# Kernel tuning notes

Hardware: AMD Instinct MI355X
Metric: run time of the kernel (lower is better)

The kernel has to match this reference:

```python
import jax, jax.numpy as jnp
import numpy as np

N, E, DIM, EDIM, H, T = 30000, 300000, 64, 16, 3, 6


def setup_inputs() -> dict:
    key = jax.random.key(0)
    ks = jax.random.split(key, 20)
    s = 0.1
    inp = {
        'x': jax.random.normal(ks[0], (N, DIM), jnp.float32),
        'edge_index': jax.random.randint(ks[1], (2, E), 0, N, jnp.int64),
        'edge_attr': jax.random.normal(ks[2], (E, EDIM), jnp.float32),
        # EdgeGATConv params (heads=3, out per head = DIM, concat=False -> head mean)
        'Wg': jax.random.normal(ks[3], (DIM, H * DIM), jnp.float32) * s,
        'bg': jnp.zeros((DIM,), jnp.float32),
        'a_src': jax.random.normal(ks[4], (H, DIM), jnp.float32) * s,
        'a_dst': jax.random.normal(ks[5], (H, DIM), jnp.float32) * s,
        'We': jax.random.normal(ks[6], (EDIM, H * DIM), jnp.float32) * s,
        'a_edge': jax.random.normal(ks[7], (H, DIM), jnp.float32) * s,
        # GRU (1 layer), torch gate order: r, z, n
        'Wih': jax.random.normal(ks[8], (3 * DIM, DIM), jnp.float32) * s,
        'Whh': jax.random.normal(ks[9], (3 * DIM, DIM), jnp.float32) * s,
        'bih': jnp.zeros((3 * DIM,), jnp.float32),
        'bhh': jnp.zeros((3 * DIM,), jnp.float32),
        # NodeLevelBatchNorm per time step
        'gamma': jnp.ones((T, DIM), jnp.float32),
        'beta': jnp.zeros((T, DIM), jnp.float32),
        # final linear: dim*(T+1) -> dim
        'Wlin': jax.random.normal(ks[10], (DIM * (T + 1), DIM), jnp.float32) * s,
        'blin': jnp.zeros((DIM,), jnp.float32),
    }
    return inp


def _edge_gat(x, edge_index, edge_attr, Wg, bg, a_src, a_dst, We, a_edge):
    n = x.shape[0]
    xw = (x @ Wg).reshape(n, H, DIM)                 # [N,H,C]
    ew = (edge_attr @ We).reshape(-1, H, DIM)        # [E,H,C]
    src, dst = edge_index[0], edge_index[1]
    logits = ((xw[src] * a_src).sum(-1)
              + (xw[dst] * a_dst).sum(-1)
              + (ew * a_edge).sum(-1))               # [E,H]
    logits = jax.nn.leaky_relu(logits, 0.2)
    # segment softmax over incoming edges per destination node
    amax = jax.ops.segment_max(logits, dst, num_segments=n)
    amax = jnp.where(jnp.isfinite(amax), amax, 0.0)
    ex = jnp.exp(logits - amax[dst])
    denom = jax.ops.segment_sum(ex, dst, num_segments=n)
    att = ex / (denom[dst] + 1e-16)                  # [E,H]
    agg = jax.ops.segment_sum(xw[src] * att[..., None], dst, num_segments=n)  # [N,H,C]
    return agg.mean(axis=1) + bg                     # concat=False: head mean


def _gru_step(m, h, Wih, Whh, bih, bhh):
    gi = m @ Wih.T + bih
    gh = h @ Whh.T + bhh
    ir, iz, inn = jnp.split(gi, 3, axis=-1)
    hr, hz, hn = jnp.split(gh, 3, axis=-1)
    r = jax.nn.sigmoid(ir + hr)
    z = jax.nn.sigmoid(iz + hz)
    nn_ = jnp.tanh(inn + r * hn)
    return (1.0 - z) * nn_ + z * h


def _node_bn(x, gamma, beta, eps=1e-5):
    mu = x.mean(axis=0)
    var = ((x - mu) ** 2).mean(axis=0)
    return (x - mu) * jax.lax.rsqrt(var + eps) * gamma + beta


def reference(x, edge_index, edge_attr, Wg, bg, a_src, a_dst, We, a_edge,
              Wih, Whh, bih, bhh, gamma, beta, Wlin, blin):
    h = x
    feats = [x]
    for i in range(T):
        m = jax.nn.celu(_edge_gat(x, edge_index, edge_attr, Wg, bg, a_src, a_dst, We, a_edge))
        h = _gru_step(m, h, Wih, Whh, bih, bhh)
        x = _node_bn(h, gamma[i], beta[i])
        feats.append(x)
    return jnp.concatenate(feats, axis=-1) @ Wlin + blin
```

## Files before the change

### kernel.cpp

```cpp
#include <hip/hip_runtime.h>
#include <math.h>

constexpr int N_ = 30000;
constexpr int E_ = 300000;
constexpr int SCB = (N_ + 255) / 256;

using f32x4  = __attribute__((ext_vector_type(4))) float;
using bf16x8 = __attribute__((ext_vector_type(8))) short;

__device__ __forceinline__ float4 ldg4(const float* p){ return *reinterpret_cast<const float4*>(p); }

__device__ __forceinline__ unsigned short f2bf(float f){
  union { float f; unsigned int u; } v; v.f = f;
  unsigned int r = v.u + 0x7FFFu + ((v.u >> 16) & 1u);
  return (unsigned short)(r >> 16);
}
__device__ __forceinline__ float bf2f(unsigned short b){
  union { unsigned int u; float f; } v; v.u = ((unsigned int)b) << 16;
  return v.f;
}
__device__ __forceinline__ float sigmoidf_(float x){ return 1.0f/(1.0f + __expf(-x)); }


__global__ void k_zero(int* __restrict__ deg){
  int i = blockIdx.x*256 + threadIdx.x;
  if (i < N_) deg[i] = 0;
}

__global__ void k_wfrag(const float* __restrict__ Wg, const float* __restrict__ Wih,
                        const float* __restrict__ Whh, const float* __restrict__ Wlin,
                        const float* __restrict__ We, const float* __restrict__ a_edge,
                        unsigned short* __restrict__ fG, unsigned short* __restrict__ fI,
                        unsigned short* __restrict__ fH, unsigned short* __restrict__ fL,
                        float* __restrict__ P){
  if (blockIdx.x == 256){
    int t = threadIdx.x; if (t >= 48) return;
    int j = t / 3, h = t % 3;
    float s = 0.f;
    for (int c = 0; c < 64; ++c) s += We[j*192 + h*64 + c] * a_edge[h*64 + c];
    P[j*3 + h] = s;
    return;
  }
  int id = blockIdx.x*256 + threadIdx.x;
  int lid, KT;
  const float* W; unsigned short* dst; int mode;
  if (id < 12288)      { lid = id;         KT = 2;  dst = fG; mode = 0; }
  else if (id < 24576) { lid = id - 12288; KT = 2;  dst = fI; mode = 1; }
  else if (id < 36864) { lid = id - 24576; KT = 2;  dst = fH; mode = 2; }
  else                 { lid = id - 36864; KT = 14; dst = fL; mode = 3; }
  int j = lid & 7, l = (lid >> 3) & 63, rest = lid >> 9;
  int kt = rest % KT, nt = rest / KT;
  int k = kt*32 + (l>>4)*8 + j;
  int n = nt*16 + (l&15);
  float v;
  if (mode == 0)      v = Wg[k*192 + n];
  else if (mode == 1) v = Wih[n*64 + k];
  else if (mode == 2) v = Whh[n*64 + k];
  else                v = Wlin[k*64 + n];
  dst[lid] = f2bf(v);
}

__global__ void k_hist(const int* __restrict__ ei, int* __restrict__ deg){
  int e = blockIdx.x*256 + threadIdx.x;
  if (e < E_) atomicAdd(&deg[ei[E_ + e]], 1);
}

__global__ void k_scanA(const int* __restrict__ deg, int* __restrict__ partial){
  int i = blockIdx.x*256 + threadIdx.x;
  int v = (i < N_) ? deg[i] : 0;
  #pragma unroll
  for (int off = 1; off < 64; off <<= 1) v += __shfl_xor(v, off);
  __shared__ int ws[4];
  if ((threadIdx.x & 63) == 0) ws[threadIdx.x >> 6] = v;
  __syncthreads();
  if (threadIdx.x == 0) partial[blockIdx.x] = ws[0] + ws[1] + ws[2] + ws[3];
}

__global__ void k_scanB(int* __restrict__ partial, int* __restrict__ row_ptr){
  __shared__ int s[128];
  int t = threadIdx.x;
  int v = (t < SCB) ? partial[t] : 0;
  s[t] = v; __syncthreads();
  for (int off = 1; off < 128; off <<= 1){
    int u = (t >= off) ? s[t-off] : 0;
    __syncthreads();
    s[t] += u;
    __syncthreads();
  }
  if (t < SCB) partial[t] = s[t] - v;
  if (t == 0) row_ptr[N_] = E_;
}

__global__ void k_scanC(const int* __restrict__ deg, const int* __restrict__ partial,
                        int* __restrict__ row_ptr, int* __restrict__ cursor){
  __shared__ int s[256];
  int t = threadIdx.x, i = blockIdx.x*256 + t;
  int v = (i < N_) ? deg[i] : 0;
  s[t] = v; __syncthreads();
  for (int off = 1; off < 256; off <<= 1){
    int u = (t >= off) ? s[t-off] : 0;
    __syncthreads();
    s[t] += u;
    __syncthreads();
  }
  int ex = s[t] - v + partial[blockIdx.x];
  if (i < N_){ row_ptr[i] = ex; cursor[i] = ex; }
}

__global__ void k_scatter(const int* __restrict__ ei, const float* __restrict__ edge_attr,
                          const float* __restrict__ P,
                          int* __restrict__ cursor, int* __restrict__ src_s,
                          float* __restrict__ el_s){
  __shared__ float sP[48];
  int t = threadIdx.x;
  if (t < 48) sP[t] = P[t];
  __syncthreads();
  int e = blockIdx.x*256 + t;
  if (e >= E_) return;
  const float* ea = edge_attr + (size_t)e*16;
  float v[16];
  #pragma unroll
  for (int q = 0; q < 4; ++q){
    float4 f = ldg4(ea + q*4);
    v[q*4+0]=f.x; v[q*4+1]=f.y; v[q*4+2]=f.z; v[q*4+3]=f.w;
  }
  float l0=0.f,l1=0.f,l2=0.f;
  #pragma unroll
  for (int j = 0; j < 16; ++j){
    l0 += v[j]*sP[j*3+0]; l1 += v[j]*sP[j*3+1]; l2 += v[j]*sP[j*3+2];
  }
  int d = ei[E_ + e];
  int p = atomicAdd(&cursor[d], 1);
  src_s[p] = ei[e];
  el_s[p*3+0] = l0; el_s[p*3+1] = l1; el_s[p*3+2] = l2;
}



__global__ __launch_bounds__(256) void k_xw(
    const float* __restrict__ hsrc,
    const float* __restrict__ bn_stats,
    const float* __restrict__ gamma, const float* __restrict__ beta,
    int gidx, int bn, int slot,
    const unsigned short* __restrict__ fG,
    const float* __restrict__ a_src, const float* __restrict__ a_dst,
    unsigned short* __restrict__ xw,
    float* __restrict__ asrc, float* __restrict__ adst,
    float* __restrict__ feats)
{
  __shared__ short sAf[8*64*8];
  __shared__ unsigned short sXW[64*196];
  __shared__ float sSc[64], sSh[64];
  const int t = threadIdx.x;
  const int row0 = blockIdx.x * 64;
  if (t < 64){
    float sc = 1.f, sh = 0.f;
    if (bn){
      float mu  = bn_stats[t] * (1.0f/30000.0f);
      float var = bn_stats[64+t] * (1.0f/30000.0f) - mu*mu;
      float rs = rsqrtf(var + 1e-5f);
      sc = gamma[gidx*64 + t] * rs;
      sh = beta[gidx*64 + t] - mu*sc;
    }
    sSc[t] = sc; sSh[t] = sh;
  }
  __syncthreads();
  {
    const int lr = t >> 4, k4 = (t & 15) * 4;
    const float sc0=sSc[k4],sc1=sSc[k4+1],sc2=sSc[k4+2],sc3=sSc[k4+3];
    const float sh0=sSh[k4],sh1=sSh[k4+1],sh2=sSh[k4+2],sh3=sSh[k4+3];
    const int kt = k4 >> 5, lanew = lr + (((k4>>3)&3)<<4), j0 = k4 & 7;
    #pragma unroll
    for (int i = 0; i < 4; ++i){
      int r = lr + i*16, gr = row0 + r;
      float4 v = make_float4(0.f,0.f,0.f,0.f);
      if (gr < N_){
        v = ldg4(hsrc + (size_t)gr*64 + k4);
        v.x = fmaf(v.x, sc0, sh0); v.y = fmaf(v.y, sc1, sh1);
        v.z = fmaf(v.z, sc2, sh2); v.w = fmaf(v.w, sc3, sh3);
        *reinterpret_cast<float4*>(feats + (size_t)gr*448 + slot*64 + k4) = v;
      }
      ushort4 pk; pk.x=f2bf(v.x); pk.y=f2bf(v.y); pk.z=f2bf(v.z); pk.w=f2bf(v.w);
      *reinterpret_cast<ushort4*>(&sAf[((i*2+kt)*64 + lanew)*8 + j0]) = pk;
    }
  }
  __syncthreads();
  const int w = t >> 6, l = t & 63, q = l >> 4, b = l & 15;
  f32x4 acc[12];
  #pragma unroll
  for (int nt = 0; nt < 12; ++nt) acc[nt] = (f32x4){0.f,0.f,0.f,0.f};
  bf16x8 a0 = *reinterpret_cast<bf16x8*>(&sAf[((w*2+0)*64 + l)*8]);
  bf16x8 a1 = *reinterpret_cast<bf16x8*>(&sAf[((w*2+1)*64 + l)*8]);
  #pragma unroll
  for (int nt = 0; nt < 12; ++nt){
    bf16x8 b0 = *reinterpret_cast<const bf16x8*>(fG + (size_t)((nt*2+0)*64 + l)*8);
    bf16x8 b1 = *reinterpret_cast<const bf16x8*>(fG + (size_t)((nt*2+1)*64 + l)*8);
    acc[nt] = __builtin_amdgcn_mfma_f32_16x16x32_bf16(a0, b0, acc[nt], 0, 0, 0);
    acc[nt] = __builtin_amdgcn_mfma_f32_16x16x32_bf16(a1, b1, acc[nt], 0, 0, 0);
  }
  float asl[3][4], adl[3][4];
  #pragma unroll
  for (int h = 0; h < 3; ++h)
    #pragma unroll
    for (int u = 0; u < 4; ++u){
      asl[h][u] = a_src[h*64 + u*16 + b];
      adl[h][u] = a_dst[h*64 + u*16 + b];
    }
  #pragma unroll
  for (int r = 0; r < 4; ++r){
    int gr = row0 + w*16 + q*4 + r;
    #pragma unroll
    for (int h = 0; h < 3; ++h){
      float s = 0.f, d = 0.f;
      #pragma unroll
      for (int u = 0; u < 4; ++u){
        s = fmaf(acc[4*h+u][r], asl[h][u], s);
        d = fmaf(acc[4*h+u][r], adl[h][u], d);
      }
      s += __shfl_xor(s,1); s += __shfl_xor(s,2); s += __shfl_xor(s,4); s += __shfl_xor(s,8);
      d += __shfl_xor(d,1); d += __shfl_xor(d,2); d += __shfl_xor(d,4); d += __shfl_xor(d,8);
      if (b == h && gr < N_){ asrc[gr*3+h] = s; adst[gr*3+h] = d; }
    }
  }
  #pragma unroll
  for (int nt = 0; nt < 12; ++nt){
    int col = nt*16 + b;
    #pragma unroll
    for (int r = 0; r < 4; ++r)
      sXW[(w*16 + q*4 + r)*196 + col] = f2bf(acc[nt][r]);
  }
  __syncthreads();
  #pragma unroll
  for (int i = 0; i < 12; ++i){
    int id = i*256 + t;
    int row = id / 48, cg = id % 48, gr = row0 + row;
    if (gr < N_){
      ushort4 pv = *reinterpret_cast<ushort4*>(&sXW[row*196 + cg*4]);
      *reinterpret_cast<ushort4*>(xw + (size_t)gr*192 + cg*4) = pv;
    }
  }
}

__global__ __launch_bounds__(256) void k_agg(
    const int* __restrict__ row_ptr, const int* __restrict__ src_s,
    const float* __restrict__ el_s,
    const float* __restrict__ asrc, const float* __restrict__ adst,
    const unsigned short* __restrict__ xw,
    const float* __restrict__ bg,
    float* __restrict__ mbuf, float* __restrict__ bn_stats)
{
  if (blockIdx.x == 0 && threadIdx.x < 128) bn_stats[threadIdx.x] = 0.f;
  int n = blockIdx.x*4 + (threadIdx.x >> 6);
  int c = threadIdx.x & 63;
  if (n >= N_) return;
  int p0 = row_ptr[n], p1 = row_ptr[n+1];
  float ad0 = adst[n*3+0], ad1 = adst[n*3+1], ad2 = adst[n*3+2];
  float m0 = -3.0e38f, m1 = -3.0e38f, m2 = -3.0e38f;
  float d0 = 0.f, d1 = 0.f, d2 = 0.f;
  float a0 = 0.f, a1 = 0.f, a2 = 0.f;
  for (int p = p0; p < p1; ++p){
    int s = src_s[p];
    float l0 = asrc[s*3+0] + ad0 + el_s[p*3+0];
    float l1 = asrc[s*3+1] + ad1 + el_s[p*3+1];
    float l2 = asrc[s*3+2] + ad2 + el_s[p*3+2];
    l0 = l0 > 0.f ? l0 : 0.2f*l0;
    l1 = l1 > 0.f ? l1 : 0.2f*l1;
    l2 = l2 > 0.f ? l2 : 0.2f*l2;
    const unsigned short* xp = xw + (size_t)s*192 + c;
    float v0 = bf2f(xp[0]), v1 = bf2f(xp[64]), v2 = bf2f(xp[128]);
    float nm, f, w;
    nm = fmaxf(m0,l0); f = __expf(m0-nm); w = __expf(l0-nm);
    d0 = d0*f + w; a0 = a0*f + w*v0; m0 = nm;
    nm = fmaxf(m1,l1); f = __expf(m1-nm); w = __expf(l1-nm);
    d1 = d1*f + w; a1 = a1*f + w*v1; m1 = nm;
    nm = fmaxf(m2,l2); f = __expf(m2-nm); w = __expf(l2-nm);
    d2 = d2*f + w; a2 = a2*f + w*v2; m2 = nm;
  }
  float mp = (a0/(d0+1e-16f) + a1/(d1+1e-16f) + a2/(d2+1e-16f)) * (1.0f/3.0f) + bg[c];
  mbuf[(size_t)n*64 + c] = mp > 0.f ? mp : (__expf(mp) - 1.0f);
}

__global__ __launch_bounds__(256) void k_gru(
    const float* __restrict__ mbuf, const float* __restrict__ hsrc,
    float* __restrict__ hbuf,
    const unsigned short* __restrict__ fI, const unsigned short* __restrict__ fH,
    const float* __restrict__ bih, const float* __restrict__ bhh,
    float* __restrict__ bn_stats)
{
  __shared__ short sMf[8*64*8];
  __shared__ short sHf[8*64*8];
  __shared__ float sH[64][68];
  __shared__ float sStat[128];
  const int t = threadIdx.x;
  const int row0 = blockIdx.x * 64;
  if (t < 128) sStat[t] = 0.f;
  {
    const int lr = t >> 4, k4 = (t & 15) * 4;
    const int kt = k4 >> 5, lanew = lr + (((k4>>3)&3)<<4), j0 = k4 & 7;
    #pragma unroll
    for (int i = 0; i < 4; ++i){
      int r = lr + i*16, gr = row0 + r;
      float4 vm = make_float4(0.f,0.f,0.f,0.f), vh = vm;
      if (gr < N_){ vm = ldg4(mbuf + (size_t)gr*64 + k4); vh = ldg4(hsrc + (size_t)gr*64 + k4); }
      ushort4 pm; pm.x=f2bf(vm.x); pm.y=f2bf(vm.y); pm.z=f2bf(vm.z); pm.w=f2bf(vm.w);
      ushort4 ph; ph.x=f2bf(vh.x); ph.y=f2bf(vh.y); ph.z=f2bf(vh.z); ph.w=f2bf(vh.w);
      *reinterpret_cast<ushort4*>(&sMf[((i*2+kt)*64 + lanew)*8 + j0]) = pm;
      *reinterpret_cast<ushort4*>(&sHf[((i*2+kt)*64 + lanew)*8 + j0]) = ph;
      sH[r][k4+0]=vh.x; sH[r][k4+1]=vh.y; sH[r][k4+2]=vh.z; sH[r][k4+3]=vh.w;
    }
  }
  __syncthreads();
  const int w = t >> 6, l = t & 63, q = l >> 4, b = l & 15;
  f32x4 aI[12], aH[12];
  #pragma unroll
  for (int nt = 0; nt < 12; ++nt){ aI[nt] = (f32x4){0.f,0.f,0.f,0.f}; aH[nt] = (f32x4){0.f,0.f,0.f,0.f}; }
  bf16x8 am0 = *reinterpret_cast<bf16x8*>(&sMf[((w*2+0)*64 + l)*8]);
  bf16x8 am1 = *reinterpret_cast<bf16x8*>(&sMf[((w*2+1)*64 + l)*8]);
  bf16x8 ah0 = *reinterpret_cast<bf16x8*>(&sHf[((w*2+0)*64 + l)*8]);
  bf16x8 ah1 = *reinterpret_cast<bf16x8*>(&sHf[((w*2+1)*64 + l)*8]);
  #pragma unroll
  for (int nt = 0; nt < 12; ++nt){
    bf16x8 bI0 = *reinterpret_cast<const bf16x8*>(fI + (size_t)((nt*2+0)*64 + l)*8);
    bf16x8 bI1 = *reinterpret_cast<const bf16x8*>(fI + (size_t)((nt*2+1)*64 + l)*8);
    bf16x8 bH0 = *reinterpret_cast<const bf16x8*>(fH + (size_t)((nt*2+0)*64 + l)*8);
    bf16x8 bH1 = *reinterpret_cast<const bf16x8*>(fH + (size_t)((nt*2+1)*64 + l)*8);
    aI[nt] = __builtin_amdgcn_mfma_f32_16x16x32_bf16(am0, bI0, aI[nt], 0, 0, 0);
    aI[nt] = __builtin_amdgcn_mfma_f32_16x16x32_bf16(am1, bI1, aI[nt], 0, 0, 0);
    aH[nt] = __builtin_amdgcn_mfma_f32_16x16x32_bf16(ah0, bH0, aH[nt], 0, 0, 0);
    aH[nt] = __builtin_amdgcn_mfma_f32_16x16x32_bf16(ah1, bH1, aH[nt], 0, 0, 0);
  }
  float s1[4] = {0.f,0.f,0.f,0.f}, s2[4] = {0.f,0.f,0.f,0.f};
  #pragma unroll
  for (int tt = 0; tt < 4; ++tt){
    int c = tt*16 + b;
    float bir = bih[c], biz = bih[64+c], bin = bih[128+c];
    float bhr = bhh[c], bhz = bhh[64+c], bhn = bhh[128+c];
    #pragma unroll
    for (int r = 0; r < 4; ++r){
      int row = w*16 + q*4 + r, gr = row0 + row;
      float rg = sigmoidf_(aI[tt][r]   + bir + aH[tt][r]   + bhr);
      float zg = sigmoidf_(aI[tt+4][r] + biz + aH[tt+4][r] + bhz);
      float ng = tanhf(aI[tt+8][r] + bin + rg*(aH[tt+8][r] + bhn));
      float ho = sH[row][c];
      float hv = (1.f - zg)*ng + zg*ho;
      if (gr < N_){
        hbuf[(size_t)gr*64 + c] = hv;
        s1[tt] += hv; s2[tt] += hv*hv;
      }
    }
  }
  #pragma unroll
  for (int tt = 0; tt < 4; ++tt){
    float v = s1[tt];
    v += __shfl_xor(v, 16); v += __shfl_xor(v, 32);
    float u = s2[tt];
    u += __shfl_xor(u, 16); u += __shfl_xor(u, 32);
    if (q == 0){
      atomicAdd(&sStat[tt*16 + b], v);
      atomicAdd(&sStat[64 + tt*16 + b], u);
    }
  }
  __syncthreads();
  if (t < 128) atomicAdd(&bn_stats[t], sStat[t]);
}

__global__ __launch_bounds__(256) void k_final(
    const float* __restrict__ feats, const float* __restrict__ hbuf,
    const float* __restrict__ bn_stats,
    const float* __restrict__ gamma, const float* __restrict__ beta,
    const unsigned short* __restrict__ fL, const float* __restrict__ blin,
    float* __restrict__ out)
{
  __shared__ short sAf[8*64*8];
  __shared__ float sSc[64], sSh[64];
  const int t = threadIdx.x;
  const int row0 = blockIdx.x * 64;
  if (t < 64){
    float mu  = bn_stats[t] * (1.0f/30000.0f);
    float var = bn_stats[64+t] * (1.0f/30000.0f) - mu*mu;
    float rs = rsqrtf(var + 1e-5f);
    float sc = gamma[5*64 + t] * rs;
    sSc[t] = sc;
    sSh[t] = beta[5*64 + t] - mu*sc;
  }
  const int w = t >> 6, l = t & 63, q = l >> 4, b = l & 15;
  const int lr = t >> 4, k4 = (t & 15) * 4;
  const int kt = k4 >> 5, lanew = lr + (((k4>>3)&3)<<4), j0 = k4 & 7;
  f32x4 acc[4];
  #pragma unroll
  for (int nt = 0; nt < 4; ++nt) acc[nt] = (f32x4){0.f,0.f,0.f,0.f};
  for (int kc = 0; kc < 7; ++kc){
    __syncthreads();
    {
      #pragma unroll
      for (int i = 0; i < 4; ++i){
        int r = lr + i*16, gr = row0 + r;
        float4 v = make_float4(0.f,0.f,0.f,0.f);
        if (gr < N_){
          if (kc < 6) v = ldg4(feats + (size_t)gr*448 + kc*64 + k4);
          else {
            v = ldg4(hbuf + (size_t)gr*64 + k4);
            v.x = fmaf(v.x, sSc[k4+0], sSh[k4+0]);
            v.y = fmaf(v.y, sSc[k4+1], sSh[k4+1]);
            v.z = fmaf(v.z, sSc[k4+2], sSh[k4+2]);
            v.w = fmaf(v.w, sSc[k4+3], sSh[k4+3]);
          }
        }
        ushort4 pk; pk.x=f2bf(v.x); pk.y=f2bf(v.y); pk.z=f2bf(v.z); pk.w=f2bf(v.w);
        *reinterpret_cast<ushort4*>(&sAf[((i*2+kt)*64 + lanew)*8 + j0]) = pk;
      }
    }
    __syncthreads();
    bf16x8 a0 = *reinterpret_cast<bf16x8*>(&sAf[((w*2+0)*64 + l)*8]);
    bf16x8 a1 = *reinterpret_cast<bf16x8*>(&sAf[((w*2+1)*64 + l)*8]);
    #pragma unroll
    for (int nt = 0; nt < 4; ++nt){
      bf16x8 b0 = *reinterpret_cast<const bf16x8*>(fL + (size_t)((nt*14 + kc*2+0)*64 + l)*8);
      bf16x8 b1 = *reinterpret_cast<const bf16x8*>(fL + (size_t)((nt*14 + kc*2+1)*64 + l)*8);
      acc[nt] = __builtin_amdgcn_mfma_f32_16x16x32_bf16(a0, b0, acc[nt], 0, 0, 0);
      acc[nt] = __builtin_amdgcn_mfma_f32_16x16x32_bf16(a1, b1, acc[nt], 0, 0, 0);
    }
  }
  #pragma unroll
  for (int nt = 0; nt < 4; ++nt){
    int col = nt*16 + b;
    float bl = blin[col];
    #pragma unroll
    for (int r = 0; r < 4; ++r){
      int gr = row0 + w*16 + q*4 + r;
      if (gr < N_) out[(size_t)gr*64 + col] = acc[nt][r] + bl;
    }
  }
}


extern "C" void kernel_launch(void* const* d_in, const int* in_sizes, int n_in,
                              void* d_out, int out_size, void* d_ws, size_t ws_size,
                              hipStream_t stream) {
  const float* x        = (const float*)d_in[0];
  const int*   ei       = (const int*)  d_in[1];
  const float* edge_attr= (const float*)d_in[2];
  const float* Wg       = (const float*)d_in[3];
  const float* bg       = (const float*)d_in[4];
  const float* a_src    = (const float*)d_in[5];
  const float* a_dst    = (const float*)d_in[6];
  const float* We       = (const float*)d_in[7];
  const float* a_edge   = (const float*)d_in[8];
  const float* Wih      = (const float*)d_in[9];
  const float* Whh      = (const float*)d_in[10];
  const float* bih      = (const float*)d_in[11];
  const float* bhh      = (const float*)d_in[12];
  const float* gamma    = (const float*)d_in[13];
  const float* beta     = (const float*)d_in[14];
  const float* Wlin     = (const float*)d_in[15];
  const float* blin     = (const float*)d_in[16];
  float* out = (float*)d_out;

  char* w = (char*)d_ws;
  auto alloc = [&](size_t bytes) -> void* {
    void* p = (void*)w;
    w += (bytes + 255) & ~(size_t)255;
    return p;
  };
  int*   row_ptr = (int*)  alloc((size_t)(N_+1)*4);
  int*   deg     = (int*)  alloc((size_t)N_*4);
  int*   cursor  = (int*)  alloc((size_t)N_*4);
  int*   partial = (int*)  alloc(128*4);
  int*   src_s   = (int*)  alloc((size_t)E_*4);
  float* el_s    = (float*)alloc((size_t)E_*3*4);
  float* Pw      = (float*)alloc(48*4);
  unsigned short* fG = (unsigned short*)alloc(12288*2);
  unsigned short* fI = (unsigned short*)alloc(12288*2);
  unsigned short* fH = (unsigned short*)alloc(12288*2);
  unsigned short* fL = (unsigned short*)alloc(28672*2);
  unsigned short* xw = (unsigned short*)alloc((size_t)N_*192*2);
  float* asrc    = (float*)alloc((size_t)N_*3*4);
  float* adst    = (float*)alloc((size_t)N_*3*4);
  float* mbuf    = (float*)alloc((size_t)N_*64*4);
  float* hbuf    = (float*)alloc((size_t)N_*64*4);
  float* feats   = (float*)alloc((size_t)N_*448*4);
  float* bn_stats= (float*)alloc(128*4);

  const int EB = (E_ + 255)/256;
  const int GEMMB = (N_ + 63)/64;

  k_zero   <<<SCB, 256, 0, stream>>>(deg);
  k_wfrag  <<<257, 256, 0, stream>>>(Wg, Wih, Whh, Wlin, We, a_edge, fG, fI, fH, fL, Pw);
  k_hist   <<<EB, 256, 0, stream>>>(ei, deg);
  k_scanA  <<<SCB, 256, 0, stream>>>(deg, partial);
  k_scanB  <<<1, 128, 0, stream>>>(partial, row_ptr);
  k_scanC  <<<SCB, 256, 0, stream>>>(deg, partial, row_ptr, cursor);
  k_scatter<<<EB, 256, 0, stream>>>(ei, edge_attr, Pw, cursor, src_s, el_s);

  for (int step = 0; step < 6; ++step){
    const float* hsrc = (step == 0) ? x : hbuf;
    k_xw <<<GEMMB, 256, 0, stream>>>(hsrc, bn_stats, gamma, beta,
                                     step-1, step > 0 ? 1 : 0, step,
                                     fG, a_src, a_dst, xw, asrc, adst, feats);
    k_agg<<<(N_+3)/4, 256, 0, stream>>>(row_ptr, src_s, el_s, asrc, adst, xw, bg,
                                        mbuf, bn_stats);
    k_gru<<<GEMMB, 256, 0, stream>>>(mbuf, hsrc, hbuf, fI, fH, bih, bhh, bn_stats);
  }
  k_final<<<GEMMB, 256, 0, stream>>>(feats, hbuf, bn_stats, gamma, beta, fL, blin, out);
}
```

Baseline: 669.0 us.

## Precompute per-edge attention weights in separate kernel, drop online softmax max

Adds a per-edge kernel that computes exp(leaky_relu(logit)) for each head once per step and stores it in a new att_s buffer; k_agg then sums the precomputed weights without the online-softmax max tracking and rescaling, and is unrolled by two edges. This removes redundant per-channel logit and exp work (previously repeated across all 64 lanes per node) and lengthens independent gather chains. It costs an extra kernel launch plus a stored dst_s and att_s array per step, and drops max subtraction, which risks overflow for large logits.

```diff
diff --git a/kernel.cpp b/kernel.cpp
--- a/kernel.cpp
+++ b/kernel.cpp
@@ -43,7 +43,7 @@
   }
   int id = blockIdx.x*256 + threadIdx.x;
   int lid, KT;
-  const float* W; unsigned short* dst; int mode;
+  unsigned short* dst; int mode;
   if (id < 12288)      { lid = id;         KT = 2;  dst = fG; mode = 0; }
   else if (id < 24576) { lid = id - 12288; KT = 2;  dst = fI; mode = 1; }
   else if (id < 36864) { lid = id - 24576; KT = 2;  dst = fH; mode = 2; }
@@ -110,7 +110,7 @@
 __global__ void k_scatter(const int* __restrict__ ei, const float* __restrict__ edge_attr,
                           const float* __restrict__ P,
                           int* __restrict__ cursor, int* __restrict__ src_s,
-                          float* __restrict__ el_s){
+                          int* __restrict__ dst_s, float* __restrict__ el_s){
   __shared__ float sP[48];
   int t = threadIdx.x;
   if (t < 48) sP[t] = P[t];
@@ -132,9 +132,9 @@
   int d = ei[E_ + e];
   int p = atomicAdd(&cursor[d], 1);
   src_s[p] = ei[e];
+  dst_s[p] = d;
   el_s[p*3+0] = l0; el_s[p*3+1] = l1; el_s[p*3+2] = l2;
 }
-
 
 
 __global__ __launch_bounds__(256) void k_xw(
@@ -241,10 +241,24 @@
   }
 }
 
+__global__ void k_att(const int* __restrict__ src_s, const int* __restrict__ dst_s,
+                      const float* __restrict__ el_s,
+                      const float* __restrict__ asrc, const float* __restrict__ adst,
+                      float* __restrict__ att_s){
+  int p = blockIdx.x*256 + threadIdx.x;
+  if (p >= E_) return;
+  int s = src_s[p], d = dst_s[p];
+  #pragma unroll
+  for (int h = 0; h < 3; ++h){
+    float l = asrc[s*3+h] + adst[d*3+h] + el_s[p*3+h];
+    l = l > 0.f ? l : 0.2f*l;
+    att_s[p*3+h] = __expf(l);
+  }
+}
+
 __global__ __launch_bounds__(256) void k_agg(
     const int* __restrict__ row_ptr, const int* __restrict__ src_s,
-    const float* __restrict__ el_s,
-    const float* __restrict__ asrc, const float* __restrict__ adst,
+    const float* __restrict__ att_s,
     const unsigned short* __restrict__ xw,
     const float* __restrict__ bg,
     float* __restrict__ mbuf, float* __restrict__ bn_stats)
@@ -254,27 +268,29 @@
   int c = threadIdx.x & 63;
   if (n >= N_) return;
   int p0 = row_ptr[n], p1 = row_ptr[n+1];
-  float ad0 = adst[n*3+0], ad1 = adst[n*3+1], ad2 = adst[n*3+2];
-  float m0 = -3.0e38f, m1 = -3.0e38f, m2 = -3.0e38f;
   float d0 = 0.f, d1 = 0.f, d2 = 0.f;
   float a0 = 0.f, a1 = 0.f, a2 = 0.f;
-  for (int p = p0; p < p1; ++p){
+  int p = p0;
+  for (; p + 2 <= p1; p += 2){
+    int sA = src_s[p], sB = src_s[p+1];
+    float wA0 = att_s[p*3+0], wA1 = att_s[p*3+1], wA2 = att_s[p*3+2];
+    float wB0 = att_s[p*3+3], wB1 = att_s[p*3+4], wB2 = att_s[p*3+5];
+    const unsigned short* xpA = xw + (size_t)sA*192 + c;
+    const unsigned short* xpB = xw + (size_t)sB*192 + c;
+    float vA0 = bf2f(xpA[0]), vA1 = bf2f(xpA[64]), vA2 = bf2f(xpA[128]);
+    float vB0 = bf2f(xpB[0]), vB1 = bf2f(xpB[64]), vB2 = bf2f(xpB[128]);
+    d0 += wA0 + wB0; d1 += wA1 + wB1; d2 += wA2 + wB2;
+    a0 = fmaf(wA0, vA0, a0); a1 = fmaf(wA1, vA1, a1); a2 = fmaf(wA2, vA2, a2);
+    a0 = fmaf(wB0, vB0, a0); a1 = fmaf(wB1, vB1, a1); a2 = fmaf(wB2, vB2, a2);
+  }
+  if (p < p1){
     int s = src_s[p];
-    float l0 = asrc[s*3+0] + ad0 + el_s[p*3+0];
-    float l1 = asrc[s*3+1] + ad1 + el_s[p*3+1];
-    float l2 = asrc[s*3+2] + ad2 + el_s[p*3+2];
-    l0 = l0 > 0.f ? l0 : 0.2f*l0;
-    l1 = l1 > 0.f ? l1 : 0.2f*l1;
-    l2 = l2 > 0.f ? l2 : 0.2f*l2;
+    float w0 = att_s[p*3+0], w1 = att_s[p*3+1], w2 = att_s[p*3+2];
     const unsigned short* xp = xw + (size_t)s*192 + c;
-    float v0 = bf2f(xp[0]), v1 = bf2f(xp[64]), v2 = bf2f(xp[128]);
-    float nm, f, w;
-    nm = fmaxf(m0,l0); f = __expf(m0-nm); w = __expf(l0-nm);
-    d0 = d0*f + w; a0 = a0*f + w*v0; m0 = nm;
-    nm = fmaxf(m1,l1); f = __expf(m1-nm); w = __expf(l1-nm);
-    d1 = d1*f + w; a1 = a1*f + w*v1; m1 = nm;
-    nm = fmaxf(m2,l2); f = __expf(m2-nm); w = __expf(l2-nm);
-    d2 = d2*f + w; a2 = a2*f + w*v2; m2 = nm;
+    d0 += w0; d1 += w1; d2 += w2;
+    a0 = fmaf(w0, bf2f(xp[0]), a0);
+    a1 = fmaf(w1, bf2f(xp[64]), a1);
+    a2 = fmaf(w2, bf2f(xp[128]), a2);
   }
   float mp = (a0/(d0+1e-16f) + a1/(d1+1e-16f) + a2/(d2+1e-16f)) * (1.0f/3.0f) + bg[c];
   mbuf[(size_t)n*64 + c] = mp > 0.f ? mp : (__expf(mp) - 1.0f);
@@ -467,7 +483,9 @@
   int*   cursor  = (int*)  alloc((size_t)N_*4);
   int*   partial = (int*)  alloc(128*4);
   int*   src_s   = (int*)  alloc((size_t)E_*4);
+  int*   dst_s   = (int*)  alloc((size_t)E_*4);
   float* el_s    = (float*)alloc((size_t)E_*3*4);
+  float* att_s   = (float*)alloc((size_t)E_*3*4);
   float* Pw      = (float*)alloc(48*4);
   unsigned short* fG = (unsigned short*)alloc(12288*2);
   unsigned short* fI = (unsigned short*)alloc(12288*2);
@@ -490,15 +508,15 @@
   k_scanA  <<<SCB, 256, 0, stream>>>(deg, partial);
   k_scanB  <<<1, 128, 0, stream>>>(partial, row_ptr);
   k_scanC  <<<SCB, 256, 0, stream>>>(deg, partial, row_ptr, cursor);
-  k_scatter<<<EB, 256, 0, stream>>>(ei, edge_attr, Pw, cursor, src_s, el_s);
+  k_scatter<<<EB, 256, 0, stream>>>(ei, edge_attr, Pw, cursor, src_s, dst_s, el_s);
 
   for (int step = 0; step < 6; ++step){
     const float* hsrc = (step == 0) ? x : hbuf;
     k_xw <<<GEMMB, 256, 0, stream>>>(hsrc, bn_stats, gamma, beta,
                                      step-1, step > 0 ? 1 : 0, step,
                                      fG, a_src, a_dst, xw, asrc, adst, feats);
-    k_agg<<<(N_+3)/4, 256, 0, stream>>>(row_ptr, src_s, el_s, asrc, adst, xw, bg,
-                                        mbuf, bn_stats);
+    k_att<<<EB, 256, 0, stream>>>(src_s, dst_s, el_s, asrc, adst, att_s);
+    k_agg<<<(N_+3)/4, 256, 0, stream>>>(row_ptr, src_s, att_s, xw, bg, mbuf, bn_stats);
     k_gru<<<GEMMB, 256, 0, stream>>>(mbuf, hsrc, hbuf, fI, fH, bih, bhh, bn_stats);
   }
   k_final<<<GEMMB, 256, 0, stream>>>(feats, hbuf, bn_stats, gamma, beta, fL, blin, out);
```

After: 586.8 us. -12.3%, faster.
